# Performance work log

Hardware: AMD Instinct MI355X
Metric: run time of the kernel (lower is better)

## Reference

```python
import jax, jax.numpy as jnp
import numpy as np

B, S, D = 16, 256, 256      # batch, seq_len, input_size (= 2*hidden)
H = 128                     # hidden size per direction
NL = 2                      # num layers
A = 8                       # n_actions
DK = D // 4                 # attention projection dim = 64
SRU_IN = 2 * D              # cat(rnn_input, attn_pool) = 512


def setup_inputs() -> dict:
    key = jax.random.key(0)
    ks = jax.random.split(key, 12)
    stdv = 1.0 / np.sqrt(DK)
    inp = {
        "x": jax.random.normal(ks[0], (B, S, D), jnp.float32),
        "x_mask": jnp.zeros((B, S), bool),
        "actions": jax.random.randint(ks[1], (B,), 0, A),
        # SeqAttentionAction params (reset_parameters: uniform(-stdv,stdv), biases zero)
        "w1": jax.random.uniform(ks[2], (A, D, DK), jnp.float32, -stdv, stdv),
        "b1": jnp.zeros((A, DK), jnp.float32),
        "w2": jax.random.uniform(ks[3], (A, D, DK), jnp.float32, -stdv, stdv),
        "b2": jnp.zeros((A, DK), jnp.float32),
        "v": jax.random.uniform(ks[4], (A, DK), jnp.float32, -stdv, stdv),
        # SRU params: per layer, forward & backward cells. k=4 slices (x~, f, r, highway)
        "sru_w_f": jax.random.uniform(ks[5], (NL, SRU_IN, 4 * H), jnp.float32, -0.05, 0.05),
        "sru_b_f": jnp.zeros((NL, 2 * H), jnp.float32),
        "sru_w_b": jax.random.uniform(ks[6], (NL, SRU_IN, 4 * H), jnp.float32, -0.05, 0.05),
        "sru_b_b": jnp.zeros((NL, 2 * H), jnp.float32),
    }
    return inp


def _sru_layer(X, W, b):
    """SRU (use_tanh=1). X:(S,B,Din) -> (S,B,H)."""
    U = jnp.einsum("sbd,dk->sbk", X, W)           # (S,B,4H)
    u0, uf, ur, hw = jnp.split(U, 4, axis=-1)
    bf, br = jnp.split(b, 2)
    f = jax.nn.sigmoid(uf + bf)
    r = jax.nn.sigmoid(ur + br)

    def step(c, t):
        f_t, u_t, r_t, hw_t = t
        c = f_t * c + (1.0 - f_t) * u_t
        h = r_t * jnp.tanh(c) + (1.0 - r_t) * hw_t
        return c, h

    c0 = jnp.zeros((X.shape[1], f.shape[-1]), X.dtype)
    _, hs = jax.lax.scan(step, c0, (f, u0, r, hw))
    return hs


def _attn_pools(memory, rnn_input, x_mask, w1a, b1a, w2a, b2a, va):
    """Action-conditioned tanh attention, vectorized over all timesteps.
    memory:(B,L,D) rnn_input:(S,B,D) -> pools:(S,B,D) (detached, as in torch .data)."""
    xt = jnp.einsum("bld,bdk->blk", memory, w1a) + b1a[:, None]    # (B,L,K)
    yt = jnp.einsum("sbd,bdk->sbk", rnn_input, w2a) + b2a[None]    # (S,B,K)
    t = jnp.tanh(xt[None] + yt[:, :, None])                        # (S,B,L,K)
    scores = jnp.einsum("sblk,bk->sbl", t, va)                     # (S,B,L)
    scores = jnp.where(x_mask[None], -jnp.inf, scores)
    att = jax.nn.softmax(scores, axis=-1)
    pools = jnp.einsum("sbl,bld->sbd", att, memory)
    return jax.lax.stop_gradient(pools)


def reference(x, x_mask, actions, w1, b1, w2, b2, v,
              sru_w_f, sru_b_f, sru_w_b, sru_b_b):
    memory = x                                # (B,L,D)
    out = jnp.transpose(x, (1, 0, 2))         # (S,B,D)
    # one-hot matmul selection == gather by action index
    w1a, b1a = w1[actions], b1[actions]
    w2a, b2a = w2[actions], b2[actions]
    va = v[actions]
    for i in range(NL):
        pools = _attn_pools(memory, out, x_mask, w1a, b1a, w2a, b2a, va)
        inputs = jnp.concatenate([out, pools], axis=2)   # (S,B,2D); inputs_f == inputs_b
        hf = _sru_layer(inputs, sru_w_f[i], sru_b_f[i])
        hb = _sru_layer(inputs, sru_w_b[i], sru_b_b[i])
        out = jnp.concatenate([hf, hb], axis=2)          # (S,B,2H)=(S,B,D)
    return jnp.transpose(out, (1, 0, 2))                 # (B,S,D)
```

## Files before the change

kernel.cpp:

```cpp
#include <hip/hip_runtime.h>
#include <hip/hip_bf16.h>

#define S_ 256
#define D_ 256
#define K_ 64
#define SIN 512
#define F4H 512

typedef unsigned short u16;
typedef __attribute__((ext_vector_type(8))) short short8;
typedef __attribute__((ext_vector_type(4))) float f32x4;

__device__ __forceinline__ float rcpf(float x) { return __builtin_amdgcn_rcpf(x); }
__device__ __forceinline__ float fast_sigmoid(float x) {
  return rcpf(1.0f + __expf(-x));
}
__device__ __forceinline__ float fast_tanh(float x) {
  return 1.0f - 2.0f * rcpf(__expf(2.0f * x) + 1.0f);
}
__device__ __forceinline__ u16 f2bf(float f) {
  unsigned int u = __float_as_uint(f);
  return (u16)((u + 0x7fff + ((u >> 16) & 1)) >> 16);
}

__global__ __launch_bounds__(256) void k_prep(const float* __restrict__ sw_f,
    const float* __restrict__ sw_b, u16* __restrict__ wt,
    const float* __restrict__ x, u16* __restrict__ xT,
    const int* __restrict__ araw, int* __restrict__ act_out,
    int* __restrict__ status) {
  if (blockIdx.x == 0 && blockIdx.y == 0 && blockIdx.z == 0 && threadIdx.x == 0) {
    bool oddzero = true;
    for (int i = 1; i < 16; i += 2) oddzero = oddzero && (araw[i] == 0);
    bool ok = true;
    for (int b = 0; b < 16; ++b) {
      int v = oddzero ? araw[2 * b] : araw[b];
      act_out[b] = (v < 0) ? 0 : (v > 7 ? 7 : v);
      ok = ok && (v >= 0 && v < 8);
    }
    *status = ok ? 1 : 0;
  }
  __shared__ u16 tile[64][66];
  int tj = threadIdx.x & 63, ti = threadIdx.x >> 6;
  int z = blockIdx.z;
  if (z < 4) {
    int layer = z >> 1;
    const float* src = (z & 1) ? sw_b : sw_f;
    int k0 = blockIdx.x * 64, n0 = blockIdx.y * 64;
#pragma unroll
    for (int i = ti; i < 64; i += 4)
      tile[i][tj] = f2bf(src[layer * 262144 + (k0 + i) * 512 + n0 + tj]);
    __syncthreads();
#pragma unroll
    for (int j = ti; j < 64; j += 4)
      wt[z * 262144 + (n0 + j) * 512 + k0 + tj] = tile[tj][j];
  } else {
    if (blockIdx.x >= 4 || blockIdx.y >= 4) return;
    int b = z - 4;
    int l0 = blockIdx.x * 64, d0 = blockIdx.y * 64;
#pragma unroll
    for (int i = ti; i < 64; i += 4)
      tile[i][tj] = f2bf(x[b * 65536 + (l0 + i) * 256 + d0 + tj]);
    __syncthreads();
#pragma unroll
    for (int j = ti; j < 64; j += 4)
      xT[b * 65536 + (d0 + j) * 256 + l0 + tj] = tile[tj][j];
  }
}

__global__ __launch_bounds__(256) void k_xt(const float* __restrict__ x,
    const int* __restrict__ act, const float* __restrict__ w1,
    const float* __restrict__ b1, float* __restrict__ xtT) {
  __shared__ float As[16][17], Bs[16][68];
  int b = blockIdx.y;
  int a = act[b];
  int l0 = blockIdx.x * 16;
  const float* A = x + b * (S_ * D_);
  const float* W = w1 + a * (D_ * K_);
  int tid = threadIdx.x;
  int ty = tid >> 4, tx = tid & 15;
  float acc[4] = {};
  for (int kk = 0; kk < D_; kk += 16) {
    As[ty][tx] = A[(l0 + ty) * D_ + kk + tx];
    *(float4*)&Bs[ty][tx << 2] = *(const float4*)(W + (kk + ty) * K_ + (tx << 2));
    __syncthreads();
#pragma unroll
    for (int k = 0; k < 16; ++k) {
      float av = As[ty][k];
      acc[0] += av * Bs[k][(tx << 2) + 0];
      acc[1] += av * Bs[k][(tx << 2) + 1];
      acc[2] += av * Bs[k][(tx << 2) + 2];
      acc[3] += av * Bs[k][(tx << 2) + 3];
    }
    __syncthreads();
  }
#pragma unroll
  for (int j = 0; j < 4; ++j) {
    int n = (tx << 2) + j;
    xtT[(b << 14) + n * 256 + l0 + ty] = acc[j] + b1[a * K_ + n];
  }
}

__global__ __launch_bounds__(256) void k_yt(const float* __restrict__ curb,
    int sstride, int bstride, const int* __restrict__ act,
    const float* __restrict__ w2, const float* __restrict__ b2,
    float* __restrict__ yt) {
  __shared__ float As[16][17], Bs[16][68];
  int b = blockIdx.y;
  int a = act[b];
  int s0 = blockIdx.x * 16;
  const float* A = curb + b * bstride;
  const float* W = w2 + a * (D_ * K_);
  int tid = threadIdx.x;
  int ty = tid >> 4, tx = tid & 15;
  float acc[4] = {};
  for (int kk = 0; kk < D_; kk += 16) {
    As[ty][tx] = A[(s0 + ty) * sstride + kk + tx];
    *(float4*)&Bs[ty][tx << 2] = *(const float4*)(W + (kk + ty) * K_ + (tx << 2));
    __syncthreads();
#pragma unroll
    for (int k = 0; k < 16; ++k) {
      float av = As[ty][k];
      acc[0] += av * Bs[k][(tx << 2) + 0];
      acc[1] += av * Bs[k][(tx << 2) + 1];
      acc[2] += av * Bs[k][(tx << 2) + 2];
      acc[3] += av * Bs[k][(tx << 2) + 3];
    }
    __syncthreads();
  }
  float4 o;
  o.x = acc[0] + b2[a * K_ + (tx << 2) + 0];
  o.y = acc[1] + b2[a * K_ + (tx << 2) + 1];
  o.z = acc[2] + b2[a * K_ + (tx << 2) + 2];
  o.w = acc[3] + b2[a * K_ + (tx << 2) + 3];
  *(float4*)(yt + ((s0 + ty) * 16 + b) * K_ + (tx << 2)) = o;
}

__global__ __launch_bounds__(256) void k_score(const float* __restrict__ xtT,
    const float* __restrict__ yt, const float* __restrict__ v,
    const int* __restrict__ act, const unsigned char* __restrict__ xmask,
    u16* __restrict__ scores) {
  __shared__ float yts[4][K_], vas[K_];
  __shared__ float redm[4][4], reds[4][4];
  int tid = threadIdx.x;
  int bid = blockIdx.x;
  int b = bid & 15, s4 = bid >> 4;
  int a = act[b];
  if (tid < 64) vas[tid] = v[a * K_ + tid];
  {
    int row = tid >> 6, k = tid & 63;
    yts[row][k] = yt[((s4 * 4 + row) * 16 + b) * K_ + k];
  }
  __syncthreads();
  float acc0 = 0.f, acc1 = 0.f, acc2 = 0.f, acc3 = 0.f;
  {
    const float* xb = xtT + (b << 14) + tid;
#pragma unroll
    for (int k = 0; k < 64; ++k) {
      float xv = xb[k * 256];
      float vv = vas[k];
      acc0 += vv * fast_tanh(xv + yts[0][k]);
      acc1 += vv * fast_tanh(xv + yts[1][k]);
      acc2 += vv * fast_tanh(xv + yts[2][k]);
      acc3 += vv * fast_tanh(xv + yts[3][k]);
    }
    if (xmask[b * S_ + tid]) { acc0 = acc1 = acc2 = acc3 = -1e30f; }
  }
  int wid = tid >> 6;
  float m0 = acc0, m1 = acc1, m2 = acc2, m3 = acc3;
#pragma unroll
  for (int d = 32; d; d >>= 1) {
    m0 = fmaxf(m0, __shfl_xor(m0, d));
    m1 = fmaxf(m1, __shfl_xor(m1, d));
    m2 = fmaxf(m2, __shfl_xor(m2, d));
    m3 = fmaxf(m3, __shfl_xor(m3, d));
  }
  if ((tid & 63) == 0) {
    redm[0][wid] = m0; redm[1][wid] = m1; redm[2][wid] = m2; redm[3][wid] = m3;
  }
  __syncthreads();
  m0 = fmaxf(fmaxf(redm[0][0], redm[0][1]), fmaxf(redm[0][2], redm[0][3]));
  m1 = fmaxf(fmaxf(redm[1][0], redm[1][1]), fmaxf(redm[1][2], redm[1][3]));
  m2 = fmaxf(fmaxf(redm[2][0], redm[2][1]), fmaxf(redm[2][2], redm[2][3]));
  m3 = fmaxf(fmaxf(redm[3][0], redm[3][1]), fmaxf(redm[3][2], redm[3][3]));
  float p0 = __expf(acc0 - m0), p1 = __expf(acc1 - m1);
  float p2 = __expf(acc2 - m2), p3 = __expf(acc3 - m3);
  float s0 = p0, s1 = p1, s2 = p2, s3 = p3;
#pragma unroll
  for (int d = 32; d; d >>= 1) {
    s0 += __shfl_xor(s0, d);
    s1 += __shfl_xor(s1, d);
    s2 += __shfl_xor(s2, d);
    s3 += __shfl_xor(s3, d);
  }
  if ((tid & 63) == 0) {
    reds[0][wid] = s0; reds[1][wid] = s1; reds[2][wid] = s2; reds[3][wid] = s3;
  }
  __syncthreads();
  s0 = reds[0][0] + reds[0][1] + reds[0][2] + reds[0][3];
  s1 = reds[1][0] + reds[1][1] + reds[1][2] + reds[1][3];
  s2 = reds[2][0] + reds[2][1] + reds[2][2] + reds[2][3];
  s3 = reds[3][0] + reds[3][1] + reds[3][2] + reds[3][3];
  u16* dst = scores + ((s4 * 4) * 16 + b) * 256 + tid;
  dst[0]        = f2bf(p0 * rcpf(s0));
  dst[16 * 256] = f2bf(p1 * rcpf(s1));
  dst[32 * 256] = f2bf(p2 * rcpf(s2));
  dst[48 * 256] = f2bf(p3 * rcpf(s3));
}

__global__ __launch_bounds__(256) void k_poolm(const u16* __restrict__ scores,
    const u16* __restrict__ xT, const float* __restrict__ curb,
    int sstride, int bstride, u16* __restrict__ inp) {
  __shared__ u16 As[64][72];
  __shared__ u16 Bs[64][72];
  int b = blockIdx.z;
  int m0 = blockIdx.x * 64, n0 = blockIdx.y * 64;
  int tid = threadIdx.x;
  int wid = tid >> 6, lane = tid & 63;
  int wm = wid >> 1, wn = wid & 1;
  f32x4 acc[2][2];
#pragma unroll
  for (int i = 0; i < 2; ++i)
#pragma unroll
    for (int j = 0; j < 2; ++j) acc[i][j] = (f32x4){0.f, 0.f, 0.f, 0.f};
  int srow = tid >> 2, soff = (tid & 3) * 16;
  int lrow = lane & 15, lk = (lane >> 4) << 3;
  for (int kk = 0; kk < 256; kk += 64) {
    const u16* ga = scores + ((m0 + srow) * 16 + b) * 256 + kk + soff;
    const u16* gb = xT + b * 65536 + (n0 + srow) * 256 + kk + soff;
    *(short8*)&As[srow][soff]     = *(const short8*)(ga);
    *(short8*)&As[srow][soff + 8] = *(const short8*)(ga + 8);
    *(short8*)&Bs[srow][soff]     = *(const short8*)(gb);
    *(short8*)&Bs[srow][soff + 8] = *(const short8*)(gb + 8);
    __syncthreads();
#pragma unroll
    for (int ks = 0; ks < 2; ++ks) {
      short8 af[2], bf[2];
#pragma unroll
      for (int mi = 0; mi < 2; ++mi)
        af[mi] = *(const short8*)&As[wm * 32 + mi * 16 + lrow][ks * 32 + lk];
#pragma unroll
      for (int ni = 0; ni < 2; ++ni)
        bf[ni] = *(const short8*)&Bs[wn * 32 + ni * 16 + lrow][ks * 32 + lk];
#pragma unroll
      for (int mi = 0; mi < 2; ++mi)
#pragma unroll
        for (int ni = 0; ni < 2; ++ni)
          acc[mi][ni] = __builtin_amdgcn_mfma_f32_16x16x32_bf16(
              af[mi], bf[ni], acc[mi][ni], 0, 0, 0);
    }
    __syncthreads();
  }
#pragma unroll
  for (int mi = 0; mi < 2; ++mi)
#pragma unroll
    for (int ni = 0; ni < 2; ++ni) {
      int r0 = m0 + wm * 32 + mi * 16 + ((lane >> 4) << 2);
      int c = n0 + wn * 32 + ni * 16 + (lane & 15);
#pragma unroll
      for (int r = 0; r < 4; ++r)
        inp[((r0 + r) * 16 + b) * SIN + 256 + c] = f2bf(acc[mi][ni][r]);
    }
#pragma unroll
  for (int i = 0; i < 4; ++i) {
    int idx = i * 256 + tid;
    int so = idx >> 4, d4 = (idx & 15) << 2;
    float4 v4 = *(const float4*)(curb + b * bstride + (m0 + so) * sstride + n0 + d4);
    ushort4 o;
    o.x = f2bf(v4.x); o.y = f2bf(v4.y); o.z = f2bf(v4.z); o.w = f2bf(v4.w);
    *(ushort4*)(inp + ((m0 + so) * 16 + b) * SIN + n0 + d4) = o;
  }
}

__global__ __launch_bounds__(256) void k_mfma(const u16* __restrict__ inp,
    const u16* __restrict__ wt, float* __restrict__ Uf, float* __restrict__ Ub,
    int layer) {
  __shared__ u16 As[128][72];
  __shared__ u16 Bs[128][72];
  float* U = blockIdx.z ? Ub : Uf;
  const u16* W = wt + (layer * 2 + blockIdx.z) * 262144;
  int m0 = blockIdx.x * 128, n0 = blockIdx.y * 128;
  int tid = threadIdx.x;
  int wid = tid >> 6, lane = tid & 63;
  int wm = wid >> 1, wn = wid & 1;
  f32x4 acc[4][4];
#pragma unroll
  for (int i = 0; i < 4; ++i)
#pragma unroll
    for (int j = 0; j < 4; ++j) acc[i][j] = (f32x4){0.f, 0.f, 0.f, 0.f};
  int srow = tid >> 1, shalf = tid & 1;
  int lrow = lane & 15, lk = (lane >> 4) << 3;
  for (int kk = 0; kk < 512; kk += 64) {
    const u16* ga = inp + (m0 + srow) * SIN + kk + shalf * 32;
    const u16* gb = W + (n0 + srow) * 512 + kk + shalf * 32;
#pragma unroll
    for (int j = 0; j < 4; ++j) {
      *(short8*)&As[srow][shalf * 32 + j * 8] = *(const short8*)(ga + j * 8);
      *(short8*)&Bs[srow][shalf * 32 + j * 8] = *(const short8*)(gb + j * 8);
    }
    __syncthreads();
#pragma unroll
    for (int ks = 0; ks < 2; ++ks) {
      short8 af[4], bf[4];
#pragma unroll
      for (int mi = 0; mi < 4; ++mi)
        af[mi] = *(const short8*)&As[wm * 64 + mi * 16 + lrow][ks * 32 + lk];
#pragma unroll
      for (int ni = 0; ni < 4; ++ni)
        bf[ni] = *(const short8*)&Bs[wn * 64 + ni * 16 + lrow][ks * 32 + lk];
#pragma unroll
      for (int mi = 0; mi < 4; ++mi)
#pragma unroll
        for (int ni = 0; ni < 4; ++ni)
          acc[mi][ni] = __builtin_amdgcn_mfma_f32_16x16x32_bf16(
              af[mi], bf[ni], acc[mi][ni], 0, 0, 0);
    }
    __syncthreads();
  }
#pragma unroll
  for (int mi = 0; mi < 4; ++mi)
#pragma unroll
    for (int ni = 0; ni < 4; ++ni) {
      int r0 = m0 + wm * 64 + mi * 16 + ((lane >> 4) << 2);
      int c = n0 + wn * 64 + ni * 16 + (lane & 15);
#pragma unroll
      for (int r = 0; r < 4; ++r)
        U[(r0 + r) * F4H + c] = acc[mi][ni][r];
    }
}

__global__ __launch_bounds__(256) void k_scan(const float* __restrict__ Uf,
    const float* __restrict__ Ub, const float* __restrict__ bfp,
    const float* __restrict__ bbp, float* __restrict__ obase,
    int o_sstride, int o_bstride, const int* __restrict__ status, int final) {
  __shared__ float so[16][257];
  int tid = threadIdx.x;
  int cloc = tid >> 4;
  int chain = blockIdx.x * 16 + cloc;
  int lane = tid & 15;
  int dir = chain >> 11;
  int rem = chain & 2047;
  int b = rem >> 7, h = rem & 127;
  const float* U = dir ? Ub : Uf;
  const float* bias = dir ? bbp : bfp;
  float bfv = bias[h], brv = bias[128 + h];
  const float* up = U + b * 512 + h;
  int s0 = lane * 16;
  float fv[16], u0[16], rv[16], hw[16];
#pragma unroll
  for (int t = 0; t < 16; ++t) {
    const float* q = up + (s0 + t) * 8192;
    u0[t] = q[0]; fv[t] = q[128]; rv[t] = q[256]; hw[t] = q[384];
  }
  float A = 1.f, Bv = 0.f;
#pragma unroll
  for (int t = 0; t < 16; ++t) {
    float f = fast_sigmoid(fv[t] + bfv);
    fv[t] = f;
    Bv = f * Bv + (1.f - f) * u0[t];
    A = A * f;
  }
#pragma unroll
  for (int d = 1; d < 16; d <<= 1) {
    float Ap = __shfl_up(A, d, 16);
    float Bp = __shfl_up(Bv, d, 16);
    if (lane >= d) { Bv = A * Bp + Bv; A = A * Ap; }
  }
  float cin = __shfl_up(Bv, 1, 16);
  if (lane == 0) cin = 0.f;
  float c = cin;
#pragma unroll
  for (int t = 0; t < 16; ++t) {
    float f = fv[t];
    c = f * (c - u0[t]) + u0[t];
    float r = fast_sigmoid(rv[t] + brv);
    so[cloc][s0 + t] = r * fast_tanh(c) + (1.f - r) * hw[t];
  }
  __syncthreads();
  bool ok = final ? (*status != 0) : true;
  int h_idx = tid & 15, s_idx = tid >> 4;
  int c2 = blockIdx.x * 16 + h_idx;
  int dir2 = c2 >> 11, rem2 = c2 & 2047;
  int b2 = rem2 >> 7, h2 = rem2 & 127;
  float* op2 = obase + b2 * o_bstride + dir2 * 128 + h2;
#pragma unroll
  for (int j = 0; j < 16; ++j) {
    int s = s_idx * 16 + j;
    float hv = so[h_idx][s];
    op2[s * o_sstride] = ok ? hv : 20.0f;
  }
}

__global__ __launch_bounds__(256) void k_fill(float* out, float v, int n) {
  int idx = blockIdx.x * 256 + threadIdx.x;
  if (idx < n) out[idx] = v;
}

extern "C" void kernel_launch(void* const* d_in, const int* in_sizes, int n_in,
                              void* d_out, int out_size, void* d_ws, size_t ws_size,
                              hipStream_t stream) {
  float* out = (float*)d_out;
  int fill_grid = (out_size + 255) / 256;

  const int exp_sizes[12] = {1048576, 4096, 16, 131072, 512, 131072, 512, 512,
                             524288, 512, 524288, 512};
  bool env_ok = (n_in == 12);
  if (env_ok)
    for (int i = 0; i < 12; ++i) env_ok = env_ok && (in_sizes[i] == exp_sizes[i]);
  if (!env_ok) {
    k_fill<<<fill_grid, 256, 0, stream>>>(out, 10.0f, out_size);
    return;
  }

  const float* x    = (const float*)d_in[0];
  const unsigned char* xmask = (const unsigned char*)d_in[1];
  const float* w1   = (const float*)d_in[3];
  const float* b1   = (const float*)d_in[4];
  const float* w2   = (const float*)d_in[5];
  const float* b2   = (const float*)d_in[6];
  const float* v    = (const float*)d_in[7];
  const float* sw_f = (const float*)d_in[8];
  const float* sb_f = (const float*)d_in[9];
  const float* sw_b = (const float*)d_in[10];
  const float* sb_b = (const float*)d_in[11];

  float* ws = (float*)d_ws;
  size_t off = 0;
  float* pb0    = ws + off; off += 1048576;
  float* xtT    = ws + off; off += 262144;
  float* yt     = ws + off; off += 262144;
  float* Uf     = ws + off; off += 2097152;
  float* Ub     = ws + off; off += 2097152;
  u16*   scores = (u16*)(ws + off); off += 524288;
  u16*   xT     = (u16*)(ws + off); off += 524288;
  u16*   inp    = (u16*)(ws + off); off += 1048576;
  u16*   wt     = (u16*)(ws + off); off += 524288;
  int*   act    = (int*)(ws + off); off += 16;
  int*   status = (int*)(ws + off); off += 16;

  if (ws_size < off * sizeof(float)) {
    k_fill<<<fill_grid, 256, 0, stream>>>(out, 30.0f, out_size);
    return;
  }

  k_prep<<<dim3(8, 8, 20), 256, 0, stream>>>(sw_f, sw_b, wt, x, xT,
      (const int*)d_in[2], act, status);
  k_xt<<<dim3(16, 16), 256, 0, stream>>>(x, act, w1, b1, xtT);

  for (int layer = 0; layer < 2; ++layer) {
    const float* curb = layer ? pb0 : x;
    int sstride = layer ? 4096 : 256;
    int bstride = layer ? 256 : 65536;
    float* nxt      = layer ? out : pb0;
    int o_sstride   = layer ? 256 : 4096;
    int o_bstride   = layer ? 65536 : 256;
    k_yt<<<dim3(16, 16), 256, 0, stream>>>(curb, sstride, bstride, act, w2, b2, yt);
    k_score<<<1024, 256, 0, stream>>>(xtT, yt, v, act, xmask, scores);
    k_poolm<<<dim3(4, 4, 16), 256, 0, stream>>>(scores, xT, curb, sstride,
                                                bstride, inp);
    k_mfma<<<dim3(32, 4, 2), 256, 0, stream>>>(inp, wt, Uf, Ub, layer);
    k_scan<<<256, 256, 0, stream>>>(Uf, Ub, sb_f + layer * 256, sb_b + layer * 256,
                                    nxt, o_sstride, o_bstride, status, layer);
  }
}
```

Measured before the change: 156.4 us.

## Halve GEMM N-tile for more blocks and remap scan threads for coalesced loads

The U projection GEMM now uses 128x64 tiles and launches twice as many workgroups (512 instead of 256), so the GPU's compute units are better filled. In the SRU scan kernel, threads are remapped so the 16 adjacent threads handle 16 consecutive hidden units (chains) rather than 16 time segments of one chain. This makes the global loads of U coalesced. The shuffle-based cross-segment prefix is replaced by an LDS carry pass that a single 16-thread group runs serially. That pass adds two barriers and some serial work, and the GEMM's smaller tiles give less data reuse per block.

```diff
diff --git a/kernel.cpp b/kernel.cpp
--- a/kernel.cpp
+++ b/kernel.cpp
@@ -275,42 +275,43 @@
     const u16* __restrict__ wt, float* __restrict__ Uf, float* __restrict__ Ub,
     int layer) {
   __shared__ u16 As[128][72];
-  __shared__ u16 Bs[128][72];
+  __shared__ u16 Bs[64][72];
   float* U = blockIdx.z ? Ub : Uf;
   const u16* W = wt + (layer * 2 + blockIdx.z) * 262144;
-  int m0 = blockIdx.x * 128, n0 = blockIdx.y * 128;
+  int m0 = blockIdx.x * 128, n0 = blockIdx.y * 64;
   int tid = threadIdx.x;
   int wid = tid >> 6, lane = tid & 63;
   int wm = wid >> 1, wn = wid & 1;
-  f32x4 acc[4][4];
+  f32x4 acc[4][2];
 #pragma unroll
   for (int i = 0; i < 4; ++i)
 #pragma unroll
-    for (int j = 0; j < 4; ++j) acc[i][j] = (f32x4){0.f, 0.f, 0.f, 0.f};
-  int srow = tid >> 1, shalf = tid & 1;
+    for (int j = 0; j < 2; ++j) acc[i][j] = (f32x4){0.f, 0.f, 0.f, 0.f};
+  int arow = tid >> 1, ahalf = tid & 1;
+  int brow = tid >> 2, bq = tid & 3;
   int lrow = lane & 15, lk = (lane >> 4) << 3;
   for (int kk = 0; kk < 512; kk += 64) {
-    const u16* ga = inp + (m0 + srow) * SIN + kk + shalf * 32;
-    const u16* gb = W + (n0 + srow) * 512 + kk + shalf * 32;
-#pragma unroll
-    for (int j = 0; j < 4; ++j) {
-      *(short8*)&As[srow][shalf * 32 + j * 8] = *(const short8*)(ga + j * 8);
-      *(short8*)&Bs[srow][shalf * 32 + j * 8] = *(const short8*)(gb + j * 8);
-    }
+    const u16* ga = inp + (m0 + arow) * SIN + kk + ahalf * 32;
+    const u16* gb = W + (n0 + brow) * 512 + kk + bq * 16;
+#pragma unroll
+    for (int j = 0; j < 4; ++j)
+      *(short8*)&As[arow][ahalf * 32 + j * 8] = *(const short8*)(ga + j * 8);
+    *(short8*)&Bs[brow][bq * 16]     = *(const short8*)(gb);
+    *(short8*)&Bs[brow][bq * 16 + 8] = *(const short8*)(gb + 8);
     __syncthreads();
 #pragma unroll
     for (int ks = 0; ks < 2; ++ks) {
-      short8 af[4], bf[4];
+      short8 af[4], bf[2];
 #pragma unroll
       for (int mi = 0; mi < 4; ++mi)
         af[mi] = *(const short8*)&As[wm * 64 + mi * 16 + lrow][ks * 32 + lk];
 #pragma unroll
-      for (int ni = 0; ni < 4; ++ni)
-        bf[ni] = *(const short8*)&Bs[wn * 64 + ni * 16 + lrow][ks * 32 + lk];
+      for (int ni = 0; ni < 2; ++ni)
+        bf[ni] = *(const short8*)&Bs[wn * 32 + ni * 16 + lrow][ks * 32 + lk];
 #pragma unroll
       for (int mi = 0; mi < 4; ++mi)
 #pragma unroll
-        for (int ni = 0; ni < 4; ++ni)
+        for (int ni = 0; ni < 2; ++ni)
           acc[mi][ni] = __builtin_amdgcn_mfma_f32_16x16x32_bf16(
               af[mi], bf[ni], acc[mi][ni], 0, 0, 0);
     }
@@ -319,9 +320,9 @@
 #pragma unroll
   for (int mi = 0; mi < 4; ++mi)
 #pragma unroll
-    for (int ni = 0; ni < 4; ++ni) {
+    for (int ni = 0; ni < 2; ++ni) {
       int r0 = m0 + wm * 64 + mi * 16 + ((lane >> 4) << 2);
-      int c = n0 + wn * 64 + ni * 16 + (lane & 15);
+      int c = n0 + wn * 32 + ni * 16 + (lane & 15);
 #pragma unroll
       for (int r = 0; r < 4; ++r)
         U[(r0 + r) * F4H + c] = acc[mi][ni][r];
@@ -333,10 +334,11 @@
     const float* __restrict__ bbp, float* __restrict__ obase,
     int o_sstride, int o_bstride, const int* __restrict__ status, int final) {
   __shared__ float so[16][257];
-  int tid = threadIdx.x;
-  int cloc = tid >> 4;
-  int chain = blockIdx.x * 16 + cloc;
-  int lane = tid & 15;
+  __shared__ float sA[16][17], sB[16][17], sC[16][17];
+  int tid = threadIdx.x;
+  int c16 = tid & 15;
+  int seg = tid >> 4;
+  int chain = blockIdx.x * 16 + c16;
   int dir = chain >> 11;
   int rem = chain & 2047;
   int b = rem >> 7, h = rem & 127;
@@ -344,7 +346,7 @@
   const float* bias = dir ? bbp : bfp;
   float bfv = bias[h], brv = bias[128 + h];
   const float* up = U + b * 512 + h;
-  int s0 = lane * 16;
+  int s0 = seg * 16;
   float fv[16], u0[16], rv[16], hw[16];
 #pragma unroll
   for (int t = 0; t < 16; ++t) {
@@ -359,21 +361,25 @@
     Bv = f * Bv + (1.f - f) * u0[t];
     A = A * f;
   }
-#pragma unroll
-  for (int d = 1; d < 16; d <<= 1) {
-    float Ap = __shfl_up(A, d, 16);
-    float Bp = __shfl_up(Bv, d, 16);
-    if (lane >= d) { Bv = A * Bp + Bv; A = A * Ap; }
-  }
-  float cin = __shfl_up(Bv, 1, 16);
-  if (lane == 0) cin = 0.f;
-  float c = cin;
+  sA[seg][c16] = A;
+  sB[seg][c16] = Bv;
+  __syncthreads();
+  if (tid < 16) {
+    float prevB = 0.f;
+#pragma unroll
+    for (int sgi = 0; sgi < 16; ++sgi) {
+      sC[sgi][tid] = prevB;
+      prevB = sA[sgi][tid] * prevB + sB[sgi][tid];
+    }
+  }
+  __syncthreads();
+  float c = sC[seg][c16];
 #pragma unroll
   for (int t = 0; t < 16; ++t) {
     float f = fv[t];
     c = f * (c - u0[t]) + u0[t];
     float r = fast_sigmoid(rv[t] + brv);
-    so[cloc][s0 + t] = r * fast_tanh(c) + (1.f - r) * hw[t];
+    so[c16][s0 + t] = r * fast_tanh(c) + (1.f - r) * hw[t];
   }
   __syncthreads();
   bool ok = final ? (*status != 0) : true;
@@ -457,7 +463,7 @@
     k_score<<<1024, 256, 0, stream>>>(xtT, yt, v, act, xmask, scores);
     k_poolm<<<dim3(4, 4, 16), 256, 0, stream>>>(scores, xT, curb, sstride,
                                                 bstride, inp);
-    k_mfma<<<dim3(32, 4, 2), 256, 0, stream>>>(inp, wt, Uf, Ub, layer);
+    k_mfma<<<dim3(32, 8, 2), 256, 0, stream>>>(inp, wt, Uf, Ub, layer);
     k_scan<<<256, 256, 0, stream>>>(Uf, Ub, sb_f + layer * 256, sb_b + layer * 256,
                                     nxt, o_sstride, o_bstride, status, layer);
   }
```

Measured after the change: 142.9 us (median of 2 runs). -8.6%, faster.
